# Kernel optimization log

Measured on AMD Instinct MI355X. Metric: run time of the kernel, lower is better.

The kernel has to match this reference:

```python
import jax, jax.numpy as jnp
import numpy as np

K = 5
EPS = 1e-08


def setup_inputs() -> dict:
    key = jax.random.key(0)
    x = jax.random.normal(key, (8192, 512), dtype=jnp.float32)
    return {"x": x}


def reference(x):
    n = x.shape[0]
    # torch: everything below through topk is under no_grad, and x is rebound
    # to the normalized tensor, so the whole graph is detached from the input.
    xn = x / jnp.linalg.norm(x, axis=1, keepdims=True)
    xn = jax.lax.stop_gradient(xn)
    dots = xn @ xn.T                                  # [N, N]
    dots = jnp.where(jnp.eye(n, dtype=bool), jnp.float32(-1.0), dots)
    _, topk_idx = jax.lax.top_k(dots, K)              # [N, K]
    x_neighbors = xn[topk_idx]                        # [N, K, D]
    diffs = xn[:, None, :] - x_neighbors              # [N, K, D]
    distances = jnp.linalg.norm(diffs, axis=-1)       # [N, K]
    mean_rho = distances.mean(axis=1)                 # [N]
    loss = -jnp.mean(jnp.log(mean_rho + EPS))
    return loss
```

## Files before the change

### kernel.cpp

```cpp
#include <hip/hip_runtime.h>
#include <math.h>

#define NROWS 8192
#define DIM   512
#define KNN   5
#define EPSV  1e-8f

#define BM 128
#define BN 128
#define BK 32
#define NT (NROWS / BM)
#define NT64 (NROWS / 64)
#define NKS (DIM / BK)
#define NWORK 2080
#define NSEL (NROWS / 4)

typedef __attribute__((ext_vector_type(8))) _Float16 f16x8;
typedef __attribute__((ext_vector_type(4))) float    f32x4;

__device__ __forceinline__ void gload16(const _Float16* g, _Float16* l) {
    __builtin_amdgcn_global_load_lds(
        (const __attribute__((address_space(1))) void*)g,
        (__attribute__((address_space(3))) void*)l, 16, 0, 0);
}

__device__ __forceinline__ void cmpswap(float& a, float& b) {
    const float hi = fmaxf(a, b), lo = fminf(a, b);
    a = hi; b = lo;
}

__device__ __forceinline__ void merge5(float a[KNN], const float b[KNN]) {
    const float c0 = fmaxf(a[0], b[0]);
    const float c1 = fmaxf(fmaxf(a[1], b[1]), fminf(a[0], b[0]));
    const float c2 = fmaxf(fmaxf(a[2], b[2]),
                           fmaxf(fminf(a[0], b[1]), fminf(a[1], b[0])));
    const float c3 = fmaxf(fmaxf(a[3], b[3]),
                           fmaxf(fminf(a[0], b[2]),
                                 fmaxf(fminf(a[1], b[1]), fminf(a[2], b[0]))));
    const float c4 = fmaxf(fmaxf(a[4], b[4]),
                           fmaxf(fmaxf(fminf(a[0], b[3]), fminf(a[1], b[2])),
                                 fmaxf(fminf(a[2], b[1]), fminf(a[3], b[0]))));
    a[0] = c0; a[1] = c1; a[2] = c2; a[3] = c3; a[4] = c4;
}

__global__ __launch_bounds__(256) void norm_kernel(const float* __restrict__ x,
                                                   _Float16* __restrict__ xnh) {
    const int wv = threadIdx.x >> 6, lane = threadIdx.x & 63;
    const int row = blockIdx.x * 4 + wv;
    const float4* xr = (const float4*)(x + (size_t)row * DIM) + lane * 2;
    const float4 a = xr[0];
    const float4 b = xr[1];
    float s = a.x * a.x + a.y * a.y + a.z * a.z + a.w * a.w
            + b.x * b.x + b.y * b.y + b.z * b.z + b.w * b.w;
    #pragma unroll
    for (int off = 1; off < 64; off <<= 1) s += __shfl_xor(s, off, 64);
    const float inv = 1.0f / sqrtf(s);
    const f16x8 h = { (_Float16)(a.x * inv), (_Float16)(a.y * inv),
                      (_Float16)(a.z * inv), (_Float16)(a.w * inv),
                      (_Float16)(b.x * inv), (_Float16)(b.y * inv),
                      (_Float16)(b.z * inv), (_Float16)(b.w * inv) };
    *(f16x8*)(xnh + (size_t)row * DIM + lane * 8) = h;
}

__global__ __launch_bounds__(256) void dots_top3_kernel(const _Float16* __restrict__ xnh,
                                                        float* __restrict__ M3) {
    int I, J;
    {
        int rem = (int)(blockIdx.x & 7) * (NWORK / 8) + (int)(blockIdx.x >> 3);
        int found = 0;
        for (int SI = 0; SI < 8 && !found; ++SI) {
            for (int SJ = SI; SJ < 8 && !found; ++SJ) {
                const int sz = (SI == SJ) ? 36 : 64;
                if (rem < sz) {
                    if (SI == SJ) {
                        int i = 0, r2 = rem;
                        while (r2 >= 8 - i) { r2 -= 8 - i; ++i; }
                        I = SI * 8 + i;
                        J = SJ * 8 + i + r2;
                    } else {
                        I = SI * 8 + (rem >> 3);
                        J = SJ * 8 + (rem & 7);
                    }
                    found = 1;
                } else {
                    rem -= sz;
                }
            }
        }
    }

    __shared__ __align__(16) _Float16 As[2][BM * BK];
    __shared__ __align__(16) _Float16 Bs[2][BN * BK];

    const int tid    = threadIdx.x;
    const int lane   = tid & 63;
    const int wv     = tid >> 6;
    const int wm     = wv >> 1;
    const int wn     = wv & 1;
    const int m_lane = lane & 15;
    const int quad   = lane >> 4;

    const int i0 = I * BM;
    const int j0 = J * BN;

    const int rowlocal = (m_lane >> 2) * 16 + quad * 4 + (m_lane & 3);
    const int myrow    = i0 + wm * 64 + rowlocal;

    const int rchunk = (quad ^ ((m_lane >> 1) & 3)) * 8;

    const int s0 = tid, s1 = tid + 256;
    const int r0g = s0 >> 2, r1g = s1 >> 2;
    const int kg0 = (s0 & 3) ^ ((s0 >> 3) & 3);
    const int kg1 = (s1 & 3) ^ ((s1 >> 3) & 3);
    const _Float16* gA0 = xnh + (size_t)(i0 + r0g) * DIM + kg0 * 8;
    const _Float16* gA1 = xnh + (size_t)(i0 + r1g) * DIM + kg1 * 8;
    const _Float16* gB0 = xnh + (size_t)(j0 + r0g) * DIM + kg0 * 8;
    const _Float16* gB1 = xnh + (size_t)(j0 + r1g) * DIM + kg1 * 8;

    f32x4 acc[4][4];
    #pragma unroll
    for (int m = 0; m < 4; ++m)
        #pragma unroll
        for (int n = 0; n < 4; ++n)
            acc[m][n] = (f32x4){0.f, 0.f, 0.f, 0.f};

    _Float16* a_cur = As[0]; _Float16* b_cur = Bs[0];
    _Float16* a_nxt = As[1]; _Float16* b_nxt = Bs[1];

    gload16(gA0, a_cur + s0 * 8);
    gload16(gA1, a_cur + s1 * 8);
    gload16(gB0, b_cur + s0 * 8);
    gload16(gB1, b_cur + s1 * 8);

    for (int ks = 0; ks < NKS; ++ks) {
        if (ks + 1 < NKS) {
            const int k0 = (ks + 1) * BK;
            gload16(gA0 + k0, a_nxt + s0 * 8);
            gload16(gA1 + k0, a_nxt + s1 * 8);
            gload16(gB0 + k0, b_nxt + s0 * 8);
            gload16(gB1 + k0, b_nxt + s1 * 8);
            asm volatile("s_waitcnt vmcnt(4)\n\ts_barrier" ::: "memory");
        } else {
            asm volatile("s_waitcnt vmcnt(0)\n\ts_barrier" ::: "memory");
        }

        f16x8 af[4], bf[4];
        #pragma unroll
        for (int m = 0; m < 4; ++m)
            af[m] = *(const f16x8*)(a_cur + (wm * 64 + m * 16 + m_lane) * BK + rchunk);
        #pragma unroll
        for (int n = 0; n < 4; ++n)
            bf[n] = *(const f16x8*)(b_cur + (wn * 64 + n * 16 + m_lane) * BK + rchunk);
        #pragma unroll
        for (int m = 0; m < 4; ++m)
            #pragma unroll
            for (int n = 0; n < 4; ++n)
                acc[m][n] = __builtin_amdgcn_mfma_f32_16x16x32_f16(af[m], bf[n], acc[m][n], 0, 0, 0);

        asm volatile("s_barrier" ::: "memory");

        _Float16* t;
        t = a_cur; a_cur = a_nxt; a_nxt = t;
        t = b_cur; b_cur = b_nxt; b_nxt = t;
    }

    const bool diag = (I == J) && (wm == wn);
    #pragma unroll
    for (int m = 0; m < 4; ++m)
        #pragma unroll
        for (int i = 0; i < 4; ++i)
            acc[m][m][i] = (diag && (quad * 4 + i) == m_lane) ? -2.f : acc[m][m][i];

    float g1 = -2.f, g2 = -2.f, g3 = -2.f;
    #pragma unroll
    for (int m = 0; m < 4; ++m) {
        #pragma unroll
        for (int i = 0; i < 4; ++i) {
            float v0 = acc[m][0][i], v1 = acc[m][1][i];
            float v2 = acc[m][2][i], v3 = acc[m][3][i];
            cmpswap(v0, v1); cmpswap(v2, v3);
            cmpswap(v0, v2); cmpswap(v1, v3);
            cmpswap(v1, v2);
            float a1 = v0, a2 = v1, a3 = v2;
            #pragma unroll
            for (int d = 1; d < 16; d <<= 1) {
                const float b1 = __shfl_xor(a1, d, 64);
                const float b2 = __shfl_xor(a2, d, 64);
                const float b3 = __shfl_xor(a3, d, 64);
                const float n1 = fmaxf(a1, b1);
                const float n2 = fmaxf(fminf(a1, b1), fmaxf(a2, b2));
                const float n3 = fmaxf(fmaxf(a3, b3),
                                       fmaxf(fminf(a1, b2), fminf(a2, b1)));
                a1 = n1; a2 = n2; a3 = n3;
            }
            const bool own = (m_lane == m * 4 + i);
            g1 = own ? a1 : g1; g2 = own ? a2 : g2; g3 = own ? a3 : g3;
        }
    }
    {
        float* p = M3 + ((size_t)myrow * NT64 + (J * 2 + wn)) * 3;
        p[0] = g1; p[1] = g2; p[2] = g3;
    }

    if (I != J) {
        #pragma unroll
        for (int n = 0; n < 4; ++n) {
            float c1 = -2.f, c2 = -2.f, c3 = -2.f;
            #pragma unroll
            for (int m = 0; m < 4; ++m)
                #pragma unroll
                for (int i = 0; i < 4; ++i) {
                    const float v  = acc[m][n][i];
                    const float u1 = fminf(c1, v);
                    c1 = fmaxf(c1, v);
                    const float u2 = fminf(c2, u1);
                    c2 = fmaxf(c2, u1);
                    c3 = fmaxf(c3, u2);
                }
            #pragma unroll
            for (int d = 16; d < 64; d <<= 1) {
                const float b1 = __shfl_xor(c1, d, 64);
                const float b2 = __shfl_xor(c2, d, 64);
                const float b3 = __shfl_xor(c3, d, 64);
                const float n2 = fmaxf(fminf(c1, b1), fmaxf(c2, b2));
                const float n3 = fmaxf(fmaxf(c3, b3),
                                       fmaxf(fminf(c1, b2), fminf(c2, b1)));
                c1 = fmaxf(c1, b1); c2 = n2; c3 = n3;
            }
            if (quad == 0) {
                const int col = j0 + wn * 64 + n * 16 + m_lane;
                float* p = M3 + ((size_t)col * NT64 + (I * 2 + wm)) * 3;
                p[0] = c1; p[1] = c2; p[2] = c3;
            }
        }
    }
}

__global__ __launch_bounds__(256) void select_loss_kernel(const _Float16* __restrict__ xnh,
                                                          const float* __restrict__ M3,
                                                          float* __restrict__ partials) {
    const int wv = threadIdx.x >> 6, lane = threadIdx.x & 63;
    const int row = blockIdx.x * 4 + wv;
    const float* p = M3 + (size_t)row * NT64 * 3 + lane * 6;
    float a[3], b[3];
    a[0] = p[0]; a[1] = p[1]; a[2] = p[2];
    b[0] = p[3]; b[1] = p[4]; b[2] = p[5];

    float t[KNN];
    {
        float c[KNN] = { a[0], a[1], a[2], -2.f, -2.f };
        const float bb[KNN] = { b[0], b[1], b[2], -2.f, -2.f };
        merge5(c, bb);
        #pragma unroll
        for (int d = 1; d < 64; d <<= 1) {
            float o[KNN];
            #pragma unroll
            for (int k = 0; k < KNN; ++k) o[k] = __shfl_xor(c[k], d, 64);
            merge5(c, o);
        }
        #pragma unroll
        for (int k = 0; k < KNN; ++k) t[k] = c[k];
    }

    const unsigned long long ba = __ballot(a[2] >= t[4]);
    const unsigned long long bb_ = __ballot(b[2] >= t[4]);
    if (ba | bb_) {
        const bool fA = (ba >> lane) & 1ull, fB = (bb_ >> lane) & 1ull;
        float c[KNN] = { fA ? -2.f : a[0], fA ? -2.f : a[1], fA ? -2.f : a[2],
                         -2.f, -2.f };
        const float b5[KNN] = { fB ? -2.f : b[0], fB ? -2.f : b[1],
                                fB ? -2.f : b[2], -2.f, -2.f };
        merge5(c, b5);
        #pragma unroll
        for (int d = 1; d < 64; d <<= 1) {
            float o[KNN];
            #pragma unroll
            for (int k = 0; k < KNN; ++k) o[k] = __shfl_xor(c[k], d, 64);
            merge5(c, o);
        }
        #pragma unroll
        for (int k = 0; k < KNN; ++k) t[k] = c[k];

        unsigned long long fl[2] = { ba, bb_ };
        #pragma unroll
        for (int h = 0; h < 2; ++h) {
            unsigned long long m = fl[h];
            while (m) {
                const int l = __ffsll((long long)m) - 1;
                m &= m - 1;
                const int jt2 = 2 * l + h;
                const int col = jt2 * 64 + lane;
                const _Float16* rp = xnh + (size_t)row * DIM;
                const _Float16* cp = xnh + (size_t)col * DIM;
                float d = 0.f;
                for (int k8 = 0; k8 < DIM / 8; ++k8) {
                    const f16x8 rv = *(const f16x8*)(rp + k8 * 8);
                    const f16x8 cv = *(const f16x8*)(cp + k8 * 8);
                    #pragma unroll
                    for (int e = 0; e < 8; ++e)
                        d += (float)rv[e] * (float)cv[e];
                }
                if (col == row) d = -2.f;
                float c2[KNN] = { d, -2.f, -2.f, -2.f, -2.f };
                #pragma unroll
                for (int dd = 1; dd < 64; dd <<= 1) {
                    float o[KNN];
                    #pragma unroll
                    for (int k = 0; k < KNN; ++k) o[k] = __shfl_xor(c2[k], dd, 64);
                    merge5(c2, o);
                }
                merge5(t, c2);
            }
        }
    }

    float s = 0.f;
    #pragma unroll
    for (int k = 0; k < KNN; ++k) s += sqrtf(fmaxf(2.f - 2.f * t[k], 0.f));
    const float val = logf(s * (1.f / KNN) + EPSV);

    __shared__ float red[4];
    if (lane == 0) red[wv] = val;
    __syncthreads();
    if (threadIdx.x == 0)
        partials[blockIdx.x] = red[0] + red[1] + red[2] + red[3];
}

__global__ __launch_bounds__(256) void reduce_kernel(const float* __restrict__ partials,
                                                     float* __restrict__ out) {
    const int tid = threadIdx.x, lane = tid & 63, wv = tid >> 6;
    float s = 0.f;
    #pragma unroll
    for (int q = 0; q < NSEL / 256; ++q) s += partials[tid + q * 256];
    #pragma unroll
    for (int off = 1; off < 64; off <<= 1) s += __shfl_xor(s, off, 64);
    __shared__ float red[4];
    if (lane == 0) red[wv] = s;
    __syncthreads();
    if (tid == 0)
        *out = -(red[0] + red[1] + red[2] + red[3]) / (float)NROWS;
}

extern "C" void kernel_launch(void* const* d_in, const int* in_sizes, int n_in,
                              void* d_out, int out_size, void* d_ws, size_t ws_size,
                              hipStream_t stream) {
    const float* x = (const float*)d_in[0];
    float* out = (float*)d_out;
    char* ws = (char*)d_ws;

    _Float16* xnh = (_Float16*)ws;
    float* M3 = (float*)(ws + (size_t)NROWS * DIM * sizeof(_Float16));
    float* partials = M3 + (size_t)NROWS * NT64 * 3;

    norm_kernel<<<NROWS / 4, 256, 0, stream>>>(x, xnh);
    dots_top3_kernel<<<NWORK, 256, 0, stream>>>(xnh, M3);
    select_loss_kernel<<<NSEL, 256, 0, stream>>>(xnh, M3, partials);
    reduce_kernel<<<1, 256, 0, stream>>>(partials, out);
}
```

Measured before the change: 158.9 us.

## Triple-buffer LDS tiles with prefetch distance two and drop trailing barrier

Moves the GEMM k-loop from double to triple buffering in LDS, issuing global-to-LDS loads two stages ahead and removing the end-of-iteration barrier, since the buffer being refilled is never the one being read. The loop is fully unrolled so buffer indices are compile-time constants. The goal is more latency hiding and one fewer barrier per k-step, in exchange for 50% more LDS per block, which may reduce occupancy.

```diff
diff --git a/kernel.cpp b/kernel.cpp
--- a/kernel.cpp
+++ b/kernel.cpp
@@ -89,8 +89,8 @@
         }
     }
 
-    __shared__ __align__(16) _Float16 As[2][BM * BK];
-    __shared__ __align__(16) _Float16 Bs[2][BN * BK];
+    __shared__ __align__(16) _Float16 As[3][BM * BK];
+    __shared__ __align__(16) _Float16 Bs[3][BN * BK];
 
     const int tid    = threadIdx.x;
     const int lane   = tid & 63;
@@ -117,6 +117,15 @@
     const _Float16* gB0 = xnh + (size_t)(j0 + r0g) * DIM + kg0 * 8;
     const _Float16* gB1 = xnh + (size_t)(j0 + r1g) * DIM + kg1 * 8;
 
+    #define STAGE(kt_, abuf_, bbuf_)                       \
+        do {                                               \
+            const int k0_ = (kt_) * BK;                    \
+            gload16(gA0 + k0_, (abuf_) + s0 * 8);          \
+            gload16(gA1 + k0_, (abuf_) + s1 * 8);          \
+            gload16(gB0 + k0_, (bbuf_) + s0 * 8);          \
+            gload16(gB1 + k0_, (bbuf_) + s1 * 8);          \
+        } while (0)
+
     f32x4 acc[4][4];
     #pragma unroll
     for (int m = 0; m < 4; ++m)
@@ -124,26 +133,20 @@
         for (int n = 0; n < 4; ++n)
             acc[m][n] = (f32x4){0.f, 0.f, 0.f, 0.f};
 
-    _Float16* a_cur = As[0]; _Float16* b_cur = Bs[0];
-    _Float16* a_nxt = As[1]; _Float16* b_nxt = Bs[1];
-
-    gload16(gA0, a_cur + s0 * 8);
-    gload16(gA1, a_cur + s1 * 8);
-    gload16(gB0, b_cur + s0 * 8);
-    gload16(gB1, b_cur + s1 * 8);
-
+    STAGE(0, As[0], Bs[0]);
+    STAGE(1, As[1], Bs[1]);
+
+    #pragma unroll
     for (int ks = 0; ks < NKS; ++ks) {
-        if (ks + 1 < NKS) {
-            const int k0 = (ks + 1) * BK;
-            gload16(gA0 + k0, a_nxt + s0 * 8);
-            gload16(gA1 + k0, a_nxt + s1 * 8);
-            gload16(gB0 + k0, b_nxt + s0 * 8);
-            gload16(gB1 + k0, b_nxt + s1 * 8);
+        if (ks < NKS - 1)
             asm volatile("s_waitcnt vmcnt(4)\n\ts_barrier" ::: "memory");
-        } else {
+        else
             asm volatile("s_waitcnt vmcnt(0)\n\ts_barrier" ::: "memory");
-        }
-
+
+        if (ks + 2 < NKS) STAGE(ks + 2, As[(ks + 2) % 3], Bs[(ks + 2) % 3]);
+
+        const _Float16* a_cur = As[ks % 3];
+        const _Float16* b_cur = Bs[ks % 3];
         f16x8 af[4], bf[4];
         #pragma unroll
         for (int m = 0; m < 4; ++m)
@@ -156,13 +159,8 @@
             #pragma unroll
             for (int n = 0; n < 4; ++n)
                 acc[m][n] = __builtin_amdgcn_mfma_f32_16x16x32_f16(af[m], bf[n], acc[m][n], 0, 0, 0);
-
-        asm volatile("s_barrier" ::: "memory");
-
-        _Float16* t;
-        t = a_cur; a_cur = a_nxt; a_nxt = t;
-        t = b_cur; b_cur = b_nxt; b_nxt = t;
-    }
+    }
+    #undef STAGE
 
     const bool diag = (I == J) && (wm == wn);
     #pragma unroll
```

Result: faster. 149.1 us (-6.1%).
